# Kernel optimization log

Measured on AMD Instinct MI355X. Metric: run time of the kernel, lower is better.

Reference implementation:

```python
import jax, jax.numpy as jnp
import numpy as np

B, N, H = 1024, 200, 64


def setup_inputs() -> dict:
    key = jax.random.key(0)
    ks = jax.random.split(key, 8)
    A = jax.random.uniform(ks[0], (B, 2 * N, N), dtype=jnp.float32)
    hidden = jax.random.normal(ks[1], (B, N, H), dtype=jnp.float32)
    s = 1.0 / np.sqrt(H)
    w_ih = jax.random.normal(ks[2], (3 * H, 2 * H), dtype=jnp.float32) * s
    w_hh = jax.random.normal(ks[3], (3 * H, H), dtype=jnp.float32) * s
    b_ih = jnp.zeros((3 * H,), jnp.float32)
    b_hh = jnp.zeros((3 * H,), jnp.float32)
    b_iah = jnp.zeros((H,), jnp.float32)
    b_oah = jnp.zeros((H,), jnp.float32)
    W_in = jax.random.normal(ks[4], (H, H), dtype=jnp.float32) * s
    bias_in = jnp.zeros((H,), jnp.float32)
    W_out = jax.random.normal(ks[5], (H, H), dtype=jnp.float32) * s
    bias_out = jnp.zeros((H,), jnp.float32)
    return {"A": A, "hidden": hidden, "w_ih": w_ih, "w_hh": w_hh,
            "b_ih": b_ih, "b_hh": b_hh, "b_iah": b_iah, "b_oah": b_oah,
            "W_in": W_in, "bias_in": bias_in, "W_out": W_out, "bias_out": bias_out}


def reference(A, hidden, w_ih, w_hh, b_ih, b_hh, b_iah, b_oah,
              W_in, bias_in, W_out, bias_out):
    # SessionGNN._cell, step=1.
    n = A.shape[1] // 2
    A_in, A_out = A[:, :n, :], A[:, n:, :]          # (B, N, N) each
    h_in = jnp.einsum('bnh,gh->bng', hidden, W_in) + bias_in    # (B, N, H)
    h_out = jnp.einsum('bnh,gh->bng', hidden, W_out) + bias_out
    input_in = jnp.matmul(A_in, h_in) + b_iah       # (B, N, H)
    input_out = jnp.matmul(A_out, h_out) + b_oah
    inputs = jnp.concatenate([input_in, input_out], axis=2)     # (B, N, 2H)
    gi = jnp.einsum('bni,gi->bng', inputs, w_ih) + b_ih         # (B, N, 3H)
    gh = jnp.einsum('bnh,gh->bng', hidden, w_hh) + b_hh
    i_r, i_i, i_n = jnp.split(gi, 3, axis=2)
    h_r, h_i, h_n = jnp.split(gh, 3, axis=2)
    resetgate = jax.nn.sigmoid(i_r + h_r)
    inputgate = jax.nn.sigmoid(i_i + h_i)
    newgate = jnp.tanh(i_n + resetgate * h_n)
    return hidden - inputgate * (hidden - newgate)
```

## Files before the change

### kernel.cpp

```cpp
#include <hip/hip_runtime.h>

typedef _Float16 f16;
typedef __attribute__((ext_vector_type(4))) _Float16 f16x4;
typedef __attribute__((ext_vector_type(8))) _Float16 f16x8;
typedef __attribute__((ext_vector_type(4))) float f32x4;

#define MFMA16(a, b, c) __builtin_amdgcn_mfma_f32_16x16x32_f16((a), (b), (c), 0, 0, 0)

__device__ __forceinline__ f16x8 cvt8(float4 a, float4 b) {
    f16x8 r;
    r[0] = (f16)a.x; r[1] = (f16)a.y; r[2] = (f16)a.z; r[3] = (f16)a.w;
    r[4] = (f16)b.x; r[5] = (f16)b.y; r[6] = (f16)b.z; r[7] = (f16)b.w;
    return r;
}

__global__ void prep_kernel(const float* __restrict__ w_ih, const float* __restrict__ w_hh,
                            const float* __restrict__ b_ih, const float* __restrict__ b_hh,
                            const float* __restrict__ b_iah, const float* __restrict__ b_oah,
                            const float* __restrict__ W_in, const float* __restrict__ bias_in,
                            const float* __restrict__ W_out, const float* __restrict__ bias_out,
                            f16* __restrict__ Wc, f16* __restrict__ Whh, f16* __restrict__ Wih,
                            float* __restrict__ cstA, float* __restrict__ cstB,
                            float* __restrict__ biasc) {
    const int gid = blockIdx.x * 256 + threadIdx.x;
    const int gstride = gridDim.x * 256;
    for (int i = gid; i < 8192; i += gstride)
        Wc[i] = (f16)(i < 4096 ? W_in[i] : W_out[i - 4096]);
    for (int i = gid; i < 12288; i += gstride) Whh[i] = (f16)w_hh[i];
    for (int i = gid; i < 24576; i += gstride) Wih[i] = (f16)w_ih[i];
    for (int job = gid; job < 768; job += gstride) {
        const int g = job >> 2, q = job & 3;
        float s = (q == 0) ? b_ih[g] : 0.0f;
        const float* wr = w_ih + g * 128 + q * 32;
        for (int i = 0; i < 32; ++i)
            s += wr[i] * ((q * 32 + i < 64) ? b_iah[q * 32 + i] : b_oah[q * 32 + i - 64]);
        atomicAdd(&cstA[g], s);
    }
    for (int g = gid; g < 192; g += gstride) cstB[g] = b_hh[g];
    for (int j = gid; j < 128; j += gstride) biasc[j] = (j < 64) ? bias_in[j] : bias_out[j - 64];
}

__global__ void zero_kernel(float* __restrict__ cstA) {
    if (threadIdx.x < 192) cstA[threadIdx.x] = 0.0f;
}

__global__ __launch_bounds__(512, 2) void gru_fused(
    const float* __restrict__ A, const float* __restrict__ hidden,
    const f16* __restrict__ Wc, const f16* __restrict__ Whh, const f16* __restrict__ Wih,
    const float* __restrict__ cstA, const float* __restrict__ cstB,
    const float* __restrict__ biasc, float* __restrict__ out) {
    __shared__ __align__(16) char lds_raw[64000];
    f16* hT  = (f16*)lds_raw;
    f16* hA  = (f16*)(lds_raw + 51200);
    f16* inp = (f16*)lds_raw;

    const int b = blockIdx.x;
    const float* Ab = A + (size_t)b * 80000;
    const float* hb = hidden + (size_t)b * 12800;
    float* ob = out + (size_t)b * 12800;

    const int tid = threadIdx.x;
    const int w   = tid >> 6;
    const int l   = tid & 63;
    const int l15 = l & 15;
    const int lg  = l >> 4;

    for (int mt = w; mt < 13; mt += 8) {
        const int m  = mt * 16 + l15;
        const int mc = m < 200 ? m : 199;
        const float* hrow = hb + mc * 64;
        float4 r0 = *(const float4*)(hrow + lg * 8);
        float4 r1 = *(const float4*)(hrow + lg * 8 + 4);
        float4 r2 = *(const float4*)(hrow + 32 + lg * 8);
        float4 r3 = *(const float4*)(hrow + 32 + lg * 8 + 4);
        f16x8 a0 = cvt8(r0, r1), a1 = cvt8(r2, r3);
        const int m0 = mt * 16 + lg * 4;
#pragma unroll
        for (int jt = 0; jt < 8; ++jt) {
            const int j = jt * 16 + l15;
            f32x4 acc = {0.f, 0.f, 0.f, 0.f};
            acc = MFMA16(a0, *(const f16x8*)(Wc + j * 64 + lg * 8), acc);
            acc = MFMA16(a1, *(const f16x8*)(Wc + j * 64 + 32 + lg * 8), acc);
            const float bc = biasc[j];
            if (m0 < 200) {
                f16x4 pk;
                pk[0] = (f16)(acc[0] + bc); pk[1] = (f16)(acc[1] + bc);
                pk[2] = (f16)(acc[2] + bc); pk[3] = (f16)(acc[3] + bc);
                *(f16x4*)(hT + j * 200 + m0) = pk;
            }
        }
    }
    __syncthreads();

    const int half = w >> 2;
    const f16* hAp = hA + half * 3200 + l15 * 200;
    const f16* hTp = hT + (w * 16 + l15) * 200;

    int s_h[4], s_row[4], s_unit[4]; bool s_act[4];
#pragma unroll
    for (int r = 0; r < 4; ++r) {
        const int idx = tid + r * 512;
        s_act[r] = idx < 1600;
        const int ic = s_act[r] ? idx : 0;
        s_h[r] = ic / 800;
        const int rem = ic % 800;
        s_row[r] = rem / 50; s_unit[r] = rem % 50;
    }

    f32x4 accC[13];
#pragma unroll
    for (int t = 0; t < 13; ++t) accC[t] = (f32x4){0.f, 0.f, 0.f, 0.f};

    {
        float4 v[4];
#pragma unroll
        for (int r = 0; r < 4; ++r) if (s_act[r]) {
            const int n = s_row[r];
            const int nc = n < 200 ? n : 199;
            v[r] = *(const float4*)(Ab + (size_t)(s_h[r] * 200 + nc) * 200 + s_unit[r] * 4);
        }
#pragma unroll
        for (int r = 0; r < 4; ++r) if (s_act[r]) {
            const int idx = tid + r * 512;
            f16x4 pk;
            pk[0] = (f16)v[r].x; pk[1] = (f16)v[r].y;
            pk[2] = (f16)v[r].z; pk[3] = (f16)v[r].w;
            *(f16x4*)(hA + idx * 4) = pk;
        }
    }
    __syncthreads();

#pragma unroll
    for (int t = 0; t < 13; ++t) {
        float4 v[4];
        if (t < 12) {
#pragma unroll
            for (int r = 0; r < 4; ++r) if (s_act[r]) {
                const int n = (t + 1) * 16 + s_row[r];
                const int nc = n < 200 ? n : 199;
                v[r] = *(const float4*)(Ab + (size_t)(s_h[r] * 200 + nc) * 200 + s_unit[r] * 4);
            }
        }
#pragma unroll
        for (int k0 = 0; k0 < 224; k0 += 32) {
            f16x8 a;
            if (k0 == 192) {
                if (lg == 0) a = *(const f16x8*)(hAp + 192);
                else {
                    f16x8 z;
#pragma unroll
                    for (int q = 0; q < 8; ++q) z[q] = (f16)0.0f;
                    a = z;
                }
            } else {
                a = *(const f16x8*)(hAp + k0 + lg * 8);
            }
            f16x8 bf = *(const f16x8*)(hTp + k0 + lg * 8);
            accC[t] = MFMA16(a, bf, accC[t]);
        }
        __syncthreads();
        if (t < 12) {
#pragma unroll
            for (int r = 0; r < 4; ++r) if (s_act[r]) {
                const int idx = tid + r * 512;
                f16x4 pk;
                pk[0] = (f16)v[r].x; pk[1] = (f16)v[r].y;
                pk[2] = (f16)v[r].z; pk[3] = (f16)v[r].w;
                *(f16x4*)(hA + idx * 4) = pk;
            }
        }
        __syncthreads();
    }

#pragma unroll
    for (int t = 0; t < 13; ++t) {
#pragma unroll
        for (int r = 0; r < 4; ++r) {
            const int n = t * 16 + lg * 4 + r;
            inp[n * 136 + w * 16 + l15] = (f16)accC[t][r];
        }
    }
    __syncthreads();

    const int c   = w & 3;
    const int wm2 = w >> 2;
    const int hcol = c * 16 + l15;
    f16x8 Wf0[4], Wf1[4], Wf2[4];
#pragma unroll
    for (int k = 0; k < 4; ++k) {
        Wf0[k] = *(const f16x8*)(Wih + (hcol      ) * 128 + k * 32 + lg * 8);
        Wf1[k] = *(const f16x8*)(Wih + (64  + hcol) * 128 + k * 32 + lg * 8);
        Wf2[k] = *(const f16x8*)(Wih + (128 + hcol) * 128 + k * 32 + lg * 8);
    }
    f16x8 Hf0[2], Hf1[2], Hf2[2];
#pragma unroll
    for (int k = 0; k < 2; ++k) {
        Hf0[k] = *(const f16x8*)(Whh + (hcol      ) * 64 + k * 32 + lg * 8);
        Hf1[k] = *(const f16x8*)(Whh + (64  + hcol) * 64 + k * 32 + lg * 8);
        Hf2[k] = *(const f16x8*)(Whh + (128 + hcol) * 64 + k * 32 + lg * 8);
    }
    const float cAr = cstA[hcol], cAi = cstA[64 + hcol], cAn = cstA[128 + hcol];
    const float cBr = cstB[hcol], cBi = cstB[64 + hcol], cBn = cstB[128 + hcol];

    for (int t = wm2; t < 13; t += 2) {
        const int n  = t * 16 + l15;
        const int nc = n < 200 ? n : 199;
        f32x4 gir = {0.f,0.f,0.f,0.f}, gii = {0.f,0.f,0.f,0.f}, gin = {0.f,0.f,0.f,0.f};
        f32x4 ghr = {0.f,0.f,0.f,0.f}, ghi = {0.f,0.f,0.f,0.f}, ghn = {0.f,0.f,0.f,0.f};
#pragma unroll
        for (int k = 0; k < 4; ++k) {
            f16x8 a = *(const f16x8*)(inp + n * 136 + k * 32 + lg * 8);
            gir = MFMA16(a, Wf0[k], gir);
            gii = MFMA16(a, Wf1[k], gii);
            gin = MFMA16(a, Wf2[k], gin);
        }
#pragma unroll
        for (int k = 0; k < 2; ++k) {
            const int h = k * 32 + lg * 8;
            float4 r0 = *(const float4*)(hb + nc * 64 + h);
            float4 r1 = *(const float4*)(hb + nc * 64 + h + 4);
            f16x8 a = cvt8(r0, r1);
            ghr = MFMA16(a, Hf0[k], ghr);
            ghi = MFMA16(a, Hf1[k], ghi);
            ghn = MFMA16(a, Hf2[k], ghn);
        }
#pragma unroll
        for (int r = 0; r < 4; ++r) {
            const int row = t * 16 + lg * 4 + r;
            if (row < 200) {
                const float hv = hb[row * 64 + hcol];
                const float xr = gir[r] + ghr[r] + cAr + cBr;
                const float xi = gii[r] + ghi[r] + cAi + cBi;
                const float rg = 1.0f / (1.0f + __expf(-xr));
                const float ig = 1.0f / (1.0f + __expf(-xi));
                const float xn = gin[r] + cAn + rg * (ghn[r] + cBn);
                const float e2 = __expf(2.0f * xn);
                const float ng = 1.0f - 2.0f / (e2 + 1.0f);
                ob[row * 64 + hcol] = hv + ig * (ng - hv);
            }
        }
    }
}

extern "C" void kernel_launch(void* const* d_in, const int* in_sizes, int n_in,
                              void* d_out, int out_size, void* d_ws, size_t ws_size,
                              hipStream_t stream) {
    const float* A        = (const float*)d_in[0];
    const float* hidden   = (const float*)d_in[1];
    const float* w_ih     = (const float*)d_in[2];
    const float* w_hh     = (const float*)d_in[3];
    const float* b_ih     = (const float*)d_in[4];
    const float* b_hh     = (const float*)d_in[5];
    const float* b_iah    = (const float*)d_in[6];
    const float* b_oah    = (const float*)d_in[7];
    const float* W_in     = (const float*)d_in[8];
    const float* bias_in  = (const float*)d_in[9];
    const float* W_out    = (const float*)d_in[10];
    const float* bias_out = (const float*)d_in[11];
    float* out = (float*)d_out;

    char* wsb = (char*)d_ws;
    f16* Wc      = (f16*)wsb;
    f16* Whh     = Wc + 8192;
    f16* Wih     = Whh + 12288;
    float* cstA  = (float*)(wsb + 90112);
    float* cstB  = cstA + 192;
    float* biasc = cstB + 192;

    zero_kernel<<<dim3(1), dim3(256), 0, stream>>>(cstA);
    prep_kernel<<<dim3(64), dim3(256), 0, stream>>>(
        w_ih, w_hh, b_ih, b_hh, b_iah, b_oah, W_in, bias_in, W_out, bias_out,
        Wc, Whh, Wih, cstA, cstB, biasc);
    gru_fused<<<dim3(1024), dim3(512), 0, stream>>>(
        A, hidden, Wc, Whh, Wih, cstA, cstB, biasc, out);
}
```

Baseline: 155.4 us.

## Split fused GRU kernel into per-half input and gate kernels

Replaces the single 512-thread-per-batch fused kernel with two kernels of 256-thread blocks, two per batch. The first kernel computes one adjacency half (in or out) into an f16 global workspace, and the second computes the GRU gates from it. The A-tile staging is double-buffered in LDS, which removes one barrier per tile, and the smaller LDS footprint allows more blocks per CU. The cost is an extra global round trip for the f16 intermediate plus one more kernel launch, and the hidden projection is recomputed per half.

```diff
diff --git a/kernel.cpp b/kernel.cpp
--- a/kernel.cpp
+++ b/kernel.cpp
@@ -44,20 +44,20 @@
     if (threadIdx.x < 192) cstA[threadIdx.x] = 0.0f;
 }
 
-__global__ __launch_bounds__(512, 2) void gru_fused(
+__global__ __launch_bounds__(256, 4) void k1_inputs(
     const float* __restrict__ A, const float* __restrict__ hidden,
-    const f16* __restrict__ Wc, const f16* __restrict__ Whh, const f16* __restrict__ Wih,
-    const float* __restrict__ cstA, const float* __restrict__ cstB,
-    const float* __restrict__ biasc, float* __restrict__ out) {
-    __shared__ __align__(16) char lds_raw[64000];
-    f16* hT  = (f16*)lds_raw;
-    f16* hA  = (f16*)(lds_raw + 51200);
-    f16* inp = (f16*)lds_raw;
-
-    const int b = blockIdx.x;
-    const float* Ab = A + (size_t)b * 80000;
+    const f16* __restrict__ Wc, const float* __restrict__ biasc,
+    f16* __restrict__ inp) {
+    __shared__ __align__(16) char lds_raw[38400];
+    f16* hTh = (f16*)lds_raw;
+    f16* hA  = (f16*)(lds_raw + 25600);
+
+    const int bid  = blockIdx.x;
+    const int b    = bid >> 1;
+    const int half = bid & 1;
+    const float* Ab = A + (size_t)b * 80000 + (size_t)half * 40000;
     const float* hb = hidden + (size_t)b * 12800;
-    float* ob = out + (size_t)b * 12800;
+    f16* ob = inp + (size_t)b * 25600 + half * 64;
 
     const int tid = threadIdx.x;
     const int w   = tid >> 6;
@@ -65,7 +65,7 @@
     const int l15 = l & 15;
     const int lg  = l >> 4;
 
-    for (int mt = w; mt < 13; mt += 8) {
+    for (int mt = w; mt < 13; mt += 4) {
         const int m  = mt * 16 + l15;
         const int mc = m < 200 ? m : 199;
         const float* hrow = hb + mc * 64;
@@ -76,8 +76,9 @@
         f16x8 a0 = cvt8(r0, r1), a1 = cvt8(r2, r3);
         const int m0 = mt * 16 + lg * 4;
 #pragma unroll
-        for (int jt = 0; jt < 8; ++jt) {
-            const int j = jt * 16 + l15;
+        for (int jt = 0; jt < 4; ++jt) {
+            const int c0 = jt * 16 + l15;
+            const int j  = half * 64 + c0;
             f32x4 acc = {0.f, 0.f, 0.f, 0.f};
             acc = MFMA16(a0, *(const f16x8*)(Wc + j * 64 + lg * 8), acc);
             acc = MFMA16(a1, *(const f16x8*)(Wc + j * 64 + 32 + lg * 8), acc);
@@ -86,25 +87,19 @@
                 f16x4 pk;
                 pk[0] = (f16)(acc[0] + bc); pk[1] = (f16)(acc[1] + bc);
                 pk[2] = (f16)(acc[2] + bc); pk[3] = (f16)(acc[3] + bc);
-                *(f16x4*)(hT + j * 200 + m0) = pk;
+                *(f16x4*)(hTh + c0 * 200 + m0) = pk;
             }
         }
     }
     __syncthreads();
 
-    const int half = w >> 2;
-    const f16* hAp = hA + half * 3200 + l15 * 200;
-    const f16* hTp = hT + (w * 16 + l15) * 200;
-
-    int s_h[4], s_row[4], s_unit[4]; bool s_act[4];
+    int s_row[4], s_unit[4]; bool s_act[4];
 #pragma unroll
     for (int r = 0; r < 4; ++r) {
-        const int idx = tid + r * 512;
-        s_act[r] = idx < 1600;
+        const int idx = tid + r * 256;
+        s_act[r] = idx < 800;
         const int ic = s_act[r] ? idx : 0;
-        s_h[r] = ic / 800;
-        const int rem = ic % 800;
-        s_row[r] = rem / 50; s_unit[r] = rem % 50;
+        s_row[r] = ic / 50; s_unit[r] = ic % 50;
     }
 
     f32x4 accC[13];
@@ -116,12 +111,11 @@
 #pragma unroll
         for (int r = 0; r < 4; ++r) if (s_act[r]) {
             const int n = s_row[r];
-            const int nc = n < 200 ? n : 199;
-            v[r] = *(const float4*)(Ab + (size_t)(s_h[r] * 200 + nc) * 200 + s_unit[r] * 4);
+            v[r] = *(const float4*)(Ab + (size_t)n * 200 + s_unit[r] * 4);
         }
 #pragma unroll
         for (int r = 0; r < 4; ++r) if (s_act[r]) {
-            const int idx = tid + r * 512;
+            const int idx = tid + r * 256;
             f16x4 pk;
             pk[0] = (f16)v[r].x; pk[1] = (f16)v[r].y;
             pk[2] = (f16)v[r].z; pk[3] = (f16)v[r].w;
@@ -130,6 +124,7 @@
     }
     __syncthreads();
 
+    const f16* hTp = hTh + (w * 16 + l15) * 200;
 #pragma unroll
     for (int t = 0; t < 13; ++t) {
         float4 v[4];
@@ -138,35 +133,33 @@
             for (int r = 0; r < 4; ++r) if (s_act[r]) {
                 const int n = (t + 1) * 16 + s_row[r];
                 const int nc = n < 200 ? n : 199;
-                v[r] = *(const float4*)(Ab + (size_t)(s_h[r] * 200 + nc) * 200 + s_unit[r] * 4);
-            }
-        }
+                v[r] = *(const float4*)(Ab + (size_t)nc * 200 + s_unit[r] * 4);
+            }
+        }
+        const f16* hAb = hA + (t & 1) * 3200 + l15 * 200;
 #pragma unroll
         for (int k0 = 0; k0 < 224; k0 += 32) {
+            const int koff = (k0 == 192) ? 192 : k0 + lg * 8;
             f16x8 a;
-            if (k0 == 192) {
-                if (lg == 0) a = *(const f16x8*)(hAp + 192);
-                else {
-                    f16x8 z;
-#pragma unroll
-                    for (int q = 0; q < 8; ++q) z[q] = (f16)0.0f;
-                    a = z;
-                }
+            if (k0 == 192 && lg != 0) {
+                f16x8 z;
+#pragma unroll
+                for (int q = 0; q < 8; ++q) z[q] = (f16)0.0f;
+                a = z;
             } else {
-                a = *(const f16x8*)(hAp + k0 + lg * 8);
-            }
-            f16x8 bf = *(const f16x8*)(hTp + k0 + lg * 8);
+                a = *(const f16x8*)(hAb + koff);
+            }
+            f16x8 bf = *(const f16x8*)(hTp + koff);
             accC[t] = MFMA16(a, bf, accC[t]);
         }
-        __syncthreads();
         if (t < 12) {
 #pragma unroll
             for (int r = 0; r < 4; ++r) if (s_act[r]) {
-                const int idx = tid + r * 512;
+                const int idx = tid + r * 256;
                 f16x4 pk;
                 pk[0] = (f16)v[r].x; pk[1] = (f16)v[r].y;
                 pk[2] = (f16)v[r].z; pk[3] = (f16)v[r].w;
-                *(f16x4*)(hA + idx * 4) = pk;
+                *(f16x4*)(hA + ((t + 1) & 1) * 3200 + idx * 4) = pk;
             }
         }
         __syncthreads();
@@ -177,14 +170,30 @@
 #pragma unroll
         for (int r = 0; r < 4; ++r) {
             const int n = t * 16 + lg * 4 + r;
-            inp[n * 136 + w * 16 + l15] = (f16)accC[t][r];
-        }
-    }
-    __syncthreads();
-
-    const int c   = w & 3;
-    const int wm2 = w >> 2;
-    const int hcol = c * 16 + l15;
+            if (n < 200) ob[n * 128 + w * 16 + l15] = (f16)accC[t][r];
+        }
+    }
+}
+
+__global__ __launch_bounds__(256, 4) void k2_gates(
+    const f16* __restrict__ inp, const float* __restrict__ hidden,
+    const f16* __restrict__ Whh, const f16* __restrict__ Wih,
+    const float* __restrict__ cstA, const float* __restrict__ cstB,
+    float* __restrict__ out) {
+    const int bid = blockIdx.x;
+    const int b   = bid >> 1;
+    const int p   = bid & 1;
+    const f16* ib = inp + (size_t)b * 25600;
+    const float* hb = hidden + (size_t)b * 12800;
+    float* ob = out + (size_t)b * 12800;
+
+    const int tid = threadIdx.x;
+    const int w   = tid >> 6;
+    const int l   = tid & 63;
+    const int l15 = l & 15;
+    const int lg  = l >> 4;
+    const int hcol = w * 16 + l15;
+
     f16x8 Wf0[4], Wf1[4], Wf2[4];
 #pragma unroll
     for (int k = 0; k < 4; ++k) {
@@ -202,14 +211,14 @@
     const float cAr = cstA[hcol], cAi = cstA[64 + hcol], cAn = cstA[128 + hcol];
     const float cBr = cstB[hcol], cBi = cstB[64 + hcol], cBn = cstB[128 + hcol];
 
-    for (int t = wm2; t < 13; t += 2) {
+    for (int t = p; t < 13; t += 2) {
         const int n  = t * 16 + l15;
         const int nc = n < 200 ? n : 199;
         f32x4 gir = {0.f,0.f,0.f,0.f}, gii = {0.f,0.f,0.f,0.f}, gin = {0.f,0.f,0.f,0.f};
         f32x4 ghr = {0.f,0.f,0.f,0.f}, ghi = {0.f,0.f,0.f,0.f}, ghn = {0.f,0.f,0.f,0.f};
 #pragma unroll
         for (int k = 0; k < 4; ++k) {
-            f16x8 a = *(const f16x8*)(inp + n * 136 + k * 32 + lg * 8);
+            f16x8 a = *(const f16x8*)(ib + nc * 128 + k * 32 + lg * 8);
             gir = MFMA16(a, Wf0[k], gir);
             gii = MFMA16(a, Wf1[k], gii);
             gin = MFMA16(a, Wf2[k], gin);
@@ -266,11 +275,12 @@
     float* cstA  = (float*)(wsb + 90112);
     float* cstB  = cstA + 192;
     float* biasc = cstB + 192;
+    f16* inp     = (f16*)(wsb + 92160);
 
     zero_kernel<<<dim3(1), dim3(256), 0, stream>>>(cstA);
     prep_kernel<<<dim3(64), dim3(256), 0, stream>>>(
         w_ih, w_hh, b_ih, b_hh, b_iah, b_oah, W_in, bias_in, W_out, bias_out,
         Wc, Whh, Wih, cstA, cstB, biasc);
-    gru_fused<<<dim3(1024), dim3(512), 0, stream>>>(
-        A, hidden, Wc, Whh, Wih, cstA, cstB, biasc, out);
-}
+    k1_inputs<<<dim3(2048), dim3(256), 0, stream>>>(A, hidden, Wc, biasc, inp);
+    k2_gates<<<dim3(2048), dim3(256), 0, stream>>>(inp, hidden, Whh, Wih, cstA, cstB, out);
+}
```

New measurement: 210.8 us. 1.36x slower.

## Keep hT fragments in registers and double-buffer A tiles through global inp

Applied to the files above, without the earlier changes.

Each wave now loads its 16-column slice of hT into registers once. That frees LDS to double-buffer A row tiles of 32 rows per step (64 rows across both halves) with a padded 202-element stride. The propagation result is written straight to a per-batch global workspace instead of being held in 13 accumulator tiles and staged through LDS. This removes the per-tile syncs and LDS bank conflicts, and it targets occupancy through smaller LDS use and launch_bounds(512,4). In exchange it adds a global write and read of the intermediate inputs, and it risks register pressure or spills under the tighter launch bound.

```diff
diff --git a/kernel.cpp b/kernel.cpp
--- a/kernel.cpp
+++ b/kernel.cpp
@@ -12,6 +12,13 @@
     r[0] = (f16)a.x; r[1] = (f16)a.y; r[2] = (f16)a.z; r[3] = (f16)a.w;
     r[4] = (f16)b.x; r[5] = (f16)b.y; r[6] = (f16)b.z; r[7] = (f16)b.w;
     return r;
+}
+
+__device__ __forceinline__ f16x8 zero8() {
+    f16x8 z;
+#pragma unroll
+    for (int q = 0; q < 8; ++q) z[q] = (f16)0.0f;
+    return z;
 }
 
 __global__ void prep_kernel(const float* __restrict__ w_ih, const float* __restrict__ w_hh,
@@ -44,19 +51,19 @@
     if (threadIdx.x < 192) cstA[threadIdx.x] = 0.0f;
 }
 
-__global__ __launch_bounds__(512, 2) void gru_fused(
+__global__ __launch_bounds__(512, 4) void gru_fused(
     const float* __restrict__ A, const float* __restrict__ hidden,
     const f16* __restrict__ Wc, const f16* __restrict__ Whh, const f16* __restrict__ Wih,
     const float* __restrict__ cstA, const float* __restrict__ cstB,
-    const float* __restrict__ biasc, float* __restrict__ out) {
-    __shared__ __align__(16) char lds_raw[64000];
-    f16* hT  = (f16*)lds_raw;
-    f16* hA  = (f16*)(lds_raw + 51200);
-    f16* inp = (f16*)lds_raw;
+    const float* __restrict__ biasc, f16* __restrict__ inp, float* __restrict__ out) {
+    __shared__ __align__(16) char lds_raw[51712];
+    f16* hT = (f16*)lds_raw;
+    f16* hA = (f16*)lds_raw;
 
     const int b = blockIdx.x;
     const float* Ab = A + (size_t)b * 80000;
     const float* hb = hidden + (size_t)b * 12800;
+    f16* ib = inp + (size_t)b * 25600;
     float* ob = out + (size_t)b * 12800;
 
     const int tid = threadIdx.x;
@@ -86,104 +93,91 @@
                 f16x4 pk;
                 pk[0] = (f16)(acc[0] + bc); pk[1] = (f16)(acc[1] + bc);
                 pk[2] = (f16)(acc[2] + bc); pk[3] = (f16)(acc[3] + bc);
-                *(f16x4*)(hT + j * 200 + m0) = pk;
+                *(f16x4*)(hT + j * 202 + m0) = pk;
             }
         }
     }
     __syncthreads();
 
-    const int half = w >> 2;
-    const f16* hAp = hA + half * 3200 + l15 * 200;
-    const f16* hTp = hT + (w * 16 + l15) * 200;
-
-    int s_h[4], s_row[4], s_unit[4]; bool s_act[4];
-#pragma unroll
-    for (int r = 0; r < 4; ++r) {
-        const int idx = tid + r * 512;
-        s_act[r] = idx < 1600;
-        const int ic = s_act[r] ? idx : 0;
-        s_h[r] = ic / 800;
-        const int rem = ic % 800;
-        s_row[r] = rem / 50; s_unit[r] = rem % 50;
-    }
-
-    f32x4 accC[13];
-#pragma unroll
-    for (int t = 0; t < 13; ++t) accC[t] = (f32x4){0.f, 0.f, 0.f, 0.f};
-
+    f16x8 Bf[7];
     {
-        float4 v[4];
-#pragma unroll
-        for (int r = 0; r < 4; ++r) if (s_act[r]) {
-            const int n = s_row[r];
-            const int nc = n < 200 ? n : 199;
-            v[r] = *(const float4*)(Ab + (size_t)(s_h[r] * 200 + nc) * 200 + s_unit[r] * 4);
-        }
-#pragma unroll
-        for (int r = 0; r < 4; ++r) if (s_act[r]) {
-            const int idx = tid + r * 512;
-            f16x4 pk;
-            pk[0] = (f16)v[r].x; pk[1] = (f16)v[r].y;
-            pk[2] = (f16)v[r].z; pk[3] = (f16)v[r].w;
-            *(f16x4*)(hA + idx * 4) = pk;
-        }
+        const f16* hTp = hT + (w * 16 + l15) * 202;
+#pragma unroll
+        for (int ks = 0; ks < 6; ++ks)
+            Bf[ks] = *(const f16x8*)(hTp + ks * 32 + lg * 8);
+        Bf[6] = (lg == 0) ? *(const f16x8*)(hTp + 192) : zero8();
     }
     __syncthreads();
 
-#pragma unroll
-    for (int t = 0; t < 13; ++t) {
-        float4 v[4];
-        if (t < 12) {
-#pragma unroll
-            for (int r = 0; r < 4; ++r) if (s_act[r]) {
-                const int n = (t + 1) * 16 + s_row[r];
-                const int nc = n < 200 ? n : 199;
-                v[r] = *(const float4*)(Ab + (size_t)(s_h[r] * 200 + nc) * 200 + s_unit[r] * 4);
-            }
-        }
-#pragma unroll
-        for (int k0 = 0; k0 < 224; k0 += 32) {
-            f16x8 a;
-            if (k0 == 192) {
-                if (lg == 0) a = *(const f16x8*)(hAp + 192);
-                else {
-                    f16x8 z;
-#pragma unroll
-                    for (int q = 0; q < 8; ++q) z[q] = (f16)0.0f;
-                    a = z;
-                }
-            } else {
-                a = *(const f16x8*)(hAp + k0 + lg * 8);
-            }
-            f16x8 bf = *(const f16x8*)(hTp + k0 + lg * 8);
-            accC[t] = MFMA16(a, bf, accC[t]);
+    const int hf = w >> 2;
+    int s_half[7], s_row[7], s_c4[7]; bool s_act[7];
+#pragma unroll
+    for (int r = 0; r < 7; ++r) {
+        const int u = tid + r * 512;
+        s_act[r] = u < 3200;
+        const int uc = s_act[r] ? u : 0;
+        s_half[r] = uc / 1600;
+        const int rem = uc % 1600;
+        s_row[r] = rem / 50; s_c4[r] = rem % 50;
+    }
+
+    float4 v[7];
+#define P2_LOADS(T)                                                               \
+    {                                                                             \
+        _Pragma("unroll")                                                         \
+        for (int r = 0; r < 7; ++r) if (s_act[r]) {                               \
+            int grow = (T) * 32 + s_row[r];                                       \
+            if (grow > 199) grow = 199;                                           \
+            v[r] = *(const float4*)(Ab + (size_t)(s_half[r] * 200 + grow) * 200   \
+                                    + s_c4[r] * 4);                               \
+        }                                                                         \
+    }
+#define P2_WRITE(BUF)                                                             \
+    {                                                                             \
+        _Pragma("unroll")                                                         \
+        for (int r = 0; r < 7; ++r) if (s_act[r]) {                               \
+            f16x4 pk;                                                             \
+            pk[0] = (f16)v[r].x; pk[1] = (f16)v[r].y;                             \
+            pk[2] = (f16)v[r].z; pk[3] = (f16)v[r].w;                             \
+            *(f16x4*)(hA + ((BUF) * 64 + s_half[r] * 32 + s_row[r]) * 202         \
+                      + s_c4[r] * 4) = pk;                                        \
+        }                                                                         \
+    }
+
+    P2_LOADS(0);
+    P2_WRITE(0);
+    P2_LOADS(1);
+    __syncthreads();
+
+    for (int t = 0; t < 7; ++t) {
+#pragma unroll
+        for (int s = 0; s < 2; ++s) {
+            if (t == 6 && s == 1) break;
+            const f16* hAp = hA + ((size_t)(t & 1) * 64 + hf * 32 + s * 16 + l15) * 202;
+            f32x4 acc = {0.f, 0.f, 0.f, 0.f};
+#pragma unroll
+            for (int ks = 0; ks < 7; ++ks) {
+                f16x8 af;
+                if (ks < 6)      af = *(const f16x8*)(hAp + ks * 32 + lg * 8);
+                else if (lg == 0) af = *(const f16x8*)(hAp + 192);
+                else              af = zero8();
+                acc = MFMA16(af, Bf[ks], acc);
+            }
+#pragma unroll
+            for (int r = 0; r < 4; ++r) {
+                const int n = t * 32 + s * 16 + lg * 4 + r;
+                if (n < 200) ib[n * 128 + w * 16 + l15] = (f16)acc[r];
+            }
+        }
+        if (t < 6) {
+            P2_WRITE((t + 1) & 1);
+            if (t < 5) P2_LOADS(t + 2);
         }
         __syncthreads();
-        if (t < 12) {
-#pragma unroll
-            for (int r = 0; r < 4; ++r) if (s_act[r]) {
-                const int idx = tid + r * 512;
-                f16x4 pk;
-                pk[0] = (f16)v[r].x; pk[1] = (f16)v[r].y;
-                pk[2] = (f16)v[r].z; pk[3] = (f16)v[r].w;
-                *(f16x4*)(hA + idx * 4) = pk;
-            }
-        }
-        __syncthreads();
-    }
-
-#pragma unroll
-    for (int t = 0; t < 13; ++t) {
-#pragma unroll
-        for (int r = 0; r < 4; ++r) {
-            const int n = t * 16 + lg * 4 + r;
-            inp[n * 136 + w * 16 + l15] = (f16)accC[t][r];
-        }
-    }
-    __syncthreads();
-
-    const int c   = w & 3;
-    const int wm2 = w >> 2;
+    }
+
+    const int c    = w & 3;
+    const int wm2  = w >> 2;
     const int hcol = c * 16 + l15;
     f16x8 Wf0[4], Wf1[4], Wf2[4];
 #pragma unroll
@@ -209,7 +203,7 @@
         f32x4 ghr = {0.f,0.f,0.f,0.f}, ghi = {0.f,0.f,0.f,0.f}, ghn = {0.f,0.f,0.f,0.f};
 #pragma unroll
         for (int k = 0; k < 4; ++k) {
-            f16x8 a = *(const f16x8*)(inp + n * 136 + k * 32 + lg * 8);
+            f16x8 a = *(const f16x8*)(ib + nc * 128 + k * 32 + lg * 8);
             gir = MFMA16(a, Wf0[k], gir);
             gii = MFMA16(a, Wf1[k], gii);
             gin = MFMA16(a, Wf2[k], gin);
@@ -266,11 +260,12 @@
     float* cstA  = (float*)(wsb + 90112);
     float* cstB  = cstA + 192;
     float* biasc = cstB + 192;
+    f16* inp     = (f16*)(wsb + 92160);
 
     zero_kernel<<<dim3(1), dim3(256), 0, stream>>>(cstA);
     prep_kernel<<<dim3(64), dim3(256), 0, stream>>>(
         w_ih, w_hh, b_ih, b_hh, b_iah, b_oah, W_in, bias_in, W_out, bias_out,
         Wc, Whh, Wih, cstA, cstB, biasc);
     gru_fused<<<dim3(1024), dim3(512), 0, stream>>>(
-        A, hidden, Wc, Whh, Wih, cstA, cstB, biasc, out);
-}
+        A, hidden, Wc, Whh, Wih, cstA, cstB, biasc, inp, out);
+}
```

New measurement: 216.9 us. +39.6%, slower.
